# Kernel optimization log

Measured on AMD Instinct MI355X. Metric: run time of the kernel, lower is better.

Reference implementation:

```python
import jax, jax.numpy as jnp
import numpy as np

B, N, C, CP, H, NQ, NK = 1, 2048, 128, 16, 8, 32, 128
DH = C // H
PAD = NK // 2 - NQ // 2  # 48
NB = N // NQ  # 64 windows


def _ln(x, gamma=None, beta=None, eps=1e-5):
    mu = jnp.mean(x, axis=-1, keepdims=True)
    var = jnp.var(x, axis=-1, keepdims=True)
    y = (x - mu) * jax.lax.rsqrt(var + eps)
    if gamma is not None:
        y = y * gamma
    if beta is not None:
        y = y + beta
    return y


def _forward(atom_single_repr, atom_single_proj, atom_pair_repr,
             gamma_s, Wg_ada, bg_ada, W_skip,
             gamma_p, beta_p, W_pair,
             Wq, Wk, Wv, Wg, bg, Wo, bo, W_out, b_out):
    # --- AdaLN(a, s): LN(a) modulated by s ---
    a_ln = _ln(atom_single_repr)                       # no affine
    s_ln = _ln(atom_single_proj, gamma_s)              # scale only
    a = jax.nn.sigmoid(s_ln @ Wg_ada + bg_ada) * a_ln + s_ln @ W_skip  # (B,N,C)

    # --- pair bias: LN + no-bias linear to heads ---
    pair_bias = _ln(atom_pair_repr, gamma_p, beta_p) @ W_pair          # (B,N,N,H)

    # --- extract_local_biases: pad key dim with -10000, take sliding blocks ---
    pb = jnp.pad(pair_bias, ((0, 0), (0, 0), (PAD, PAD), (0, 0)),
                 constant_values=-10000.0)                              # (B,N,N+2P,H)
    rows = pb.reshape(B, NB, NQ, N + 2 * PAD, H)
    col_idx = (jnp.arange(NB) * NQ)[:, None] + jnp.arange(NK)[None, :]  # (NB,NK)
    local_bias = jnp.take_along_axis(rows, col_idx[None, :, None, :, None], axis=3)
    bias = jnp.transpose(local_bias, (0, 1, 4, 2, 3))                   # (B,NB,H,NQ,NK)

    # --- partition_tensor for queries (stride==size, no pad) and keys/values ---
    q_x = a.reshape(B, NB, NQ, C)
    a_pad = jnp.pad(a, ((0, 0), (PAD, PAD), (0, 0)))
    kv_x = a_pad[:, col_idx, :]                                         # (B,NB,NK,C)

    # --- OpenFold-style gated attention per window ---
    q = (q_x @ Wq).reshape(B, NB, NQ, H, DH) * (DH ** -0.5)
    k = (kv_x @ Wk).reshape(B, NB, NK, H, DH)
    v = (kv_x @ Wv).reshape(B, NB, NK, H, DH)
    logits = jnp.einsum('bwqhd,bwkhd->bwhqk', q, k) + bias
    attn = jax.nn.softmax(logits, axis=-1)
    o = jnp.einsum('bwhqk,bwkhd->bwqhd', attn, v).reshape(B, NB, NQ, C)
    g = jax.nn.sigmoid(q_x @ Wg + bg)
    o = (o * g) @ Wo + bo                                               # (B,NB,NQ,C)
    out = o.reshape(B, N, C)

    # --- output gating ---
    return jax.nn.sigmoid(out @ W_out + b_out) * out


def setup_inputs() -> dict:
    key = jax.random.key(0)
    ks = jax.random.split(key, 16)
    s = 0.02
    return {
        'atom_single_repr': jax.random.normal(ks[0], (B, N, C), jnp.float32),
        'atom_single_proj': jax.random.normal(ks[1], (B, N, C), jnp.float32),
        'atom_pair_repr': jax.random.normal(ks[2], (B, N, N, CP), jnp.float32),
        'gamma_s': jnp.ones((C,), jnp.float32),
        'Wg_ada': s * jax.random.normal(ks[3], (C, C), jnp.float32),
        'bg_ada': jnp.zeros((C,), jnp.float32),
        'W_skip': s * jax.random.normal(ks[4], (C, C), jnp.float32),
        'gamma_p': jnp.ones((CP,), jnp.float32),
        'beta_p': jnp.zeros((CP,), jnp.float32),
        'W_pair': s * jax.random.normal(ks[5], (CP, H), jnp.float32),
        'Wq': s * jax.random.normal(ks[6], (C, C), jnp.float32),
        'Wk': s * jax.random.normal(ks[7], (C, C), jnp.float32),
        'Wv': s * jax.random.normal(ks[8], (C, C), jnp.float32),
        'Wg': s * jax.random.normal(ks[9], (C, C), jnp.float32),
        'bg': jnp.ones((C,), jnp.float32),
        'Wo': s * jax.random.normal(ks[10], (C, C), jnp.float32),
        'bo': jnp.zeros((C,), jnp.float32),
        'W_out': s * jax.random.normal(ks[11], (C, C), jnp.float32),
        'b_out': -2.0 * jnp.ones((C,), jnp.float32),
    }


def reference(atom_single_repr, atom_single_proj, atom_pair_repr,
              gamma_s, Wg_ada, bg_ada, W_skip, gamma_p, beta_p, W_pair,
              Wq, Wk, Wv, Wg, bg, Wo, bo, W_out, b_out):
    return _forward(atom_single_repr, atom_single_proj, atom_pair_repr,
                    gamma_s, Wg_ada, bg_ada, W_skip, gamma_p, beta_p, W_pair,
                    Wq, Wk, Wv, Wg, bg, Wo, bo, W_out, b_out)
```

## Files before the change

kernel.cpp:

```cpp
#include <hip/hip_runtime.h>
#include <math.h>

#define NTOK 2048
#define CC   128
#define CPP  16
#define HH   8
#define DHH  16
#define NQW  32
#define NKW  128
#define PADW 48
#define NBW  64

__device__ __forceinline__ float sigm(float x) { return 1.0f / (1.0f + expf(-x)); }

__global__ __launch_bounds__(256) void k1_fused(
    const float* __restrict__ x1, const float* __restrict__ x2,
    const float* __restrict__ gamma_s,
    const float* __restrict__ Wg_ada, const float* __restrict__ bg_ada,
    const float* __restrict__ W_skip,
    const float* __restrict__ Wq, const float* __restrict__ Wk,
    const float* __restrict__ Wv, const float* __restrict__ Wg,
    const float* __restrict__ bg,
    const float* __restrict__ pair,
    const float* __restrict__ gamma_p, const float* __restrict__ beta_p,
    const float* __restrict__ W_pair,
    float* __restrict__ qb, float* __restrict__ kb,
    float* __restrict__ vb, float* __restrict__ gb,
    float* __restrict__ bias)
{
  const int b   = blockIdx.x;
  const int tid = threadIdx.x;

  if (b < 256) {
    __shared__ float sln[8][132];
    __shared__ float aln[8][132];
    __shared__ float as_[8][132];
    const int r0 = b * 8;

    {
      const int r = tid >> 5, t = tid & 31, c0 = t * 4;
      const int row = r0 + r;
      float4 v1 = *(const float4*)(x1 + (size_t)row * CC + c0);
      float4 v2 = *(const float4*)(x2 + (size_t)row * CC + c0);
      float s1 = v1.x + v1.y + v1.z + v1.w;
      float p1 = v1.x * v1.x + v1.y * v1.y + v1.z * v1.z + v1.w * v1.w;
      float s2 = v2.x + v2.y + v2.z + v2.w;
      float p2 = v2.x * v2.x + v2.y * v2.y + v2.z * v2.z + v2.w * v2.w;
#pragma unroll
      for (int m = 1; m < 32; m <<= 1) {
        s1 += __shfl_xor(s1, m); p1 += __shfl_xor(p1, m);
        s2 += __shfl_xor(s2, m); p2 += __shfl_xor(p2, m);
      }
      const float rc = 1.0f / 128.0f;
      float mu1 = s1 * rc, mu2 = s2 * rc;
      float rs1 = rsqrtf(p1 * rc - mu1 * mu1 + 1e-5f);
      float rs2 = rsqrtf(p2 * rc - mu2 * mu2 + 1e-5f);
      float4 gs = *(const float4*)(gamma_s + c0);
      float4 al, sl;
      al.x = (v1.x - mu1) * rs1; al.y = (v1.y - mu1) * rs1;
      al.z = (v1.z - mu1) * rs1; al.w = (v1.w - mu1) * rs1;
      sl.x = (v2.x - mu2) * rs2 * gs.x; sl.y = (v2.y - mu2) * rs2 * gs.y;
      sl.z = (v2.z - mu2) * rs2 * gs.z; sl.w = (v2.w - mu2) * rs2 * gs.w;
      *(float4*)(&aln[r][c0]) = al;
      *(float4*)(&sln[r][c0]) = sl;
    }
    __syncthreads();

    {
      const int rh = tid >> 7, cg = tid & 127;
      float g0 = 0.f, g1 = 0.f, g2 = 0.f, g3 = 0.f;
      float s0 = 0.f, s1 = 0.f, s2 = 0.f, s3 = 0.f;
#pragma unroll 4
      for (int k4 = 0; k4 < 32; ++k4) {
        float4 a0 = *(const float4*)(&sln[rh * 4 + 0][k4 * 4]);
        float4 a1 = *(const float4*)(&sln[rh * 4 + 1][k4 * 4]);
        float4 a2 = *(const float4*)(&sln[rh * 4 + 2][k4 * 4]);
        float4 a3 = *(const float4*)(&sln[rh * 4 + 3][k4 * 4]);
#define S1STEP(AX, J) { \
        float wg = Wg_ada[(k4 * 4 + J) * CC + cg]; \
        float wk = W_skip[(k4 * 4 + J) * CC + cg]; \
        g0 = fmaf(a0.AX, wg, g0); g1 = fmaf(a1.AX, wg, g1); \
        g2 = fmaf(a2.AX, wg, g2); g3 = fmaf(a3.AX, wg, g3); \
        s0 = fmaf(a0.AX, wk, s0); s1 = fmaf(a1.AX, wk, s1); \
        s2 = fmaf(a2.AX, wk, s2); s3 = fmaf(a3.AX, wk, s3); }
        S1STEP(x, 0) S1STEP(y, 1) S1STEP(z, 2) S1STEP(w, 3)
#undef S1STEP
      }
      float bga = bg_ada[cg];
      as_[rh * 4 + 0][cg] = sigm(g0 + bga) * aln[rh * 4 + 0][cg] + s0;
      as_[rh * 4 + 1][cg] = sigm(g1 + bga) * aln[rh * 4 + 1][cg] + s1;
      as_[rh * 4 + 2][cg] = sigm(g2 + bga) * aln[rh * 4 + 2][cg] + s2;
      as_[rh * 4 + 3][cg] = sigm(g3 + bga) * aln[rh * 4 + 3][cg] + s3;
    }
    __syncthreads();

    {
      const int m  = tid >> 6;
      const int l  = tid & 63;
      const int c0 = l * 2;
      const float* Wm = (m == 0) ? Wq : (m == 1) ? Wk : (m == 2) ? Wv : Wg;
      float2 c0_ = {0.f, 0.f}, c1_ = {0.f, 0.f}, c2_ = {0.f, 0.f}, c3_ = {0.f, 0.f};
      float2 c4_ = {0.f, 0.f}, c5_ = {0.f, 0.f}, c6_ = {0.f, 0.f}, c7_ = {0.f, 0.f};
#pragma unroll 2
      for (int k4 = 0; k4 < 32; ++k4) {
        float4 ra0 = *(const float4*)(&as_[0][k4 * 4]);
        float4 ra1 = *(const float4*)(&as_[1][k4 * 4]);
        float4 ra2 = *(const float4*)(&as_[2][k4 * 4]);
        float4 ra3 = *(const float4*)(&as_[3][k4 * 4]);
        float4 ra4 = *(const float4*)(&as_[4][k4 * 4]);
        float4 ra5 = *(const float4*)(&as_[5][k4 * 4]);
        float4 ra6 = *(const float4*)(&as_[6][k4 * 4]);
        float4 ra7 = *(const float4*)(&as_[7][k4 * 4]);
#define PJSTEP(AX, J) { \
        float2 wv = *(const float2*)(Wm + (k4 * 4 + J) * CC + c0); \
        c0_.x = fmaf(ra0.AX, wv.x, c0_.x); c0_.y = fmaf(ra0.AX, wv.y, c0_.y); \
        c1_.x = fmaf(ra1.AX, wv.x, c1_.x); c1_.y = fmaf(ra1.AX, wv.y, c1_.y); \
        c2_.x = fmaf(ra2.AX, wv.x, c2_.x); c2_.y = fmaf(ra2.AX, wv.y, c2_.y); \
        c3_.x = fmaf(ra3.AX, wv.x, c3_.x); c3_.y = fmaf(ra3.AX, wv.y, c3_.y); \
        c4_.x = fmaf(ra4.AX, wv.x, c4_.x); c4_.y = fmaf(ra4.AX, wv.y, c4_.y); \
        c5_.x = fmaf(ra5.AX, wv.x, c5_.x); c5_.y = fmaf(ra5.AX, wv.y, c5_.y); \
        c6_.x = fmaf(ra6.AX, wv.x, c6_.x); c6_.y = fmaf(ra6.AX, wv.y, c6_.y); \
        c7_.x = fmaf(ra7.AX, wv.x, c7_.x); c7_.y = fmaf(ra7.AX, wv.y, c7_.y); }
        PJSTEP(x, 0) PJSTEP(y, 1) PJSTEP(z, 2) PJSTEP(w, 3)
#undef PJSTEP
      }
      if (m == 0) {
#define QST(I, CI) { float2 r; r.x = CI.x * 0.25f; r.y = CI.y * 0.25f; \
        *(float2*)(qb + (size_t)(r0 + I) * CC + c0) = r; }
        QST(0, c0_) QST(1, c1_) QST(2, c2_) QST(3, c3_)
        QST(4, c4_) QST(5, c5_) QST(6, c6_) QST(7, c7_)
#undef QST
      } else if (m == 1) {
#define KST(I, CI) *(float2*)(kb + (size_t)(r0 + I) * CC + c0) = CI;
        KST(0, c0_) KST(1, c1_) KST(2, c2_) KST(3, c3_)
        KST(4, c4_) KST(5, c5_) KST(6, c6_) KST(7, c7_)
#undef KST
      } else if (m == 2) {
#define VST(I, CI) *(float2*)(vb + (size_t)(r0 + I) * CC + c0) = CI;
        VST(0, c0_) VST(1, c1_) VST(2, c2_) VST(3, c3_)
        VST(4, c4_) VST(5, c5_) VST(6, c6_) VST(7, c7_)
#undef VST
      } else {
        float2 bgv = *(const float2*)(bg + c0);
#define GST(I, CI) { float2 r; r.x = sigm(CI.x + bgv.x); r.y = sigm(CI.y + bgv.y); \
        *(float2*)(gb + (size_t)(r0 + I) * CC + c0) = r; }
        GST(0, c0_) GST(1, c1_) GST(2, c2_) GST(3, c3_)
        GST(4, c4_) GST(5, c5_) GST(6, c6_) GST(7, c7_)
#undef GST
      }
    }
  } else {
    __shared__ float wp[CPP * HH];
    __shared__ float gp[CPP];
    __shared__ float bp[CPP];
    if (tid < CPP * HH) wp[tid] = W_pair[tid];
    if (tid < CPP) { gp[tid] = gamma_p[tid]; bp[tid] = beta_p[tid]; }
    __syncthreads();

    const int i  = (b - 256) * 2 + (tid >> 7);
    const int w  = i >> 5;
    const int qq = i & 31;
    const int k  = tid & 127;
    const int j  = w * NQW + k - PADW;

    float bh[HH];
    if (j >= 0 && j < NTOK) {
      const float* p = pair + ((size_t)i * NTOK + j) * CPP;
      float x[CPP];
#pragma unroll
      for (int u = 0; u < CPP; u += 4) {
        float4 v = *(const float4*)(p + u);
        x[u] = v.x; x[u + 1] = v.y; x[u + 2] = v.z; x[u + 3] = v.w;
      }
      float s = 0.f;
#pragma unroll
      for (int c = 0; c < CPP; ++c) s += x[c];
      float mu = s * (1.0f / CPP);
      float vv = 0.f;
#pragma unroll
      for (int c = 0; c < CPP; ++c) { float d = x[c] - mu; vv = fmaf(d, d, vv); }
      float rs = rsqrtf(vv * (1.0f / CPP) + 1e-5f);
#pragma unroll
      for (int h = 0; h < HH; ++h) bh[h] = 0.f;
#pragma unroll
      for (int c = 0; c < CPP; ++c) {
        float y = (x[c] - mu) * rs * gp[c] + bp[c];
#pragma unroll
        for (int h = 0; h < HH; ++h) bh[h] = fmaf(y, wp[c * HH + h], bh[h]);
      }
    } else {
#pragma unroll
      for (int h = 0; h < HH; ++h) bh[h] = -10000.0f;
    }
#pragma unroll
    for (int h = 0; h < HH; ++h)
      bias[((size_t)((w * HH + h) * NQW + qq)) * NKW + k] = bh[h];
  }
}

__global__ __launch_bounds__(256) void attn_kernel(
    const float* __restrict__ qb, const float* __restrict__ kb,
    const float* __restrict__ vb, const float* __restrict__ bias,
    float* __restrict__ ob)
{
  __shared__ float qs[16][20];
  __shared__ float ks[NKW][20];
  __shared__ float vs[NKW][20];
  __shared__ float bs[16][132];
  const int u   = blockIdx.x;
  const int w   = u >> 4;
  const int h   = (u >> 1) & 7;
  const int qh  = u & 1;
  const int tid = threadIdx.x;

  if (tid < 64) {
    int qr = tid >> 2, c4 = (tid & 3) * 4;
    float4 v = *(const float4*)(qb + (size_t)(w * NQW + qh * 16 + qr) * CC + h * DHH + c4);
    *(float4*)(&qs[qr][c4]) = v;
  }
  {
    int kr = tid >> 1, c8 = (tid & 1) * 8;
    int j = w * NQW + kr - PADW;
    float4 k0 = make_float4(0.f, 0.f, 0.f, 0.f), k1 = k0, v0 = k0, v1 = k0;
    if (j >= 0 && j < NTOK) {
      const float* kp = kb + (size_t)j * CC + h * DHH + c8;
      const float* vp = vb + (size_t)j * CC + h * DHH + c8;
      k0 = *(const float4*)(kp);     k1 = *(const float4*)(kp + 4);
      v0 = *(const float4*)(vp);     v1 = *(const float4*)(vp + 4);
    }
    *(float4*)(&ks[kr][c8])     = k0;
    *(float4*)(&ks[kr][c8 + 4]) = k1;
    *(float4*)(&vs[kr][c8])     = v0;
    *(float4*)(&vs[kr][c8 + 4]) = v1;
  }
  {
    const float* bt = bias + (size_t)(w * HH + h) * NQW * NKW + (size_t)qh * 16 * NKW;
    int qr = tid >> 4, k8 = (tid & 15) * 8;
    float4 b0 = *(const float4*)(bt + qr * NKW + k8);
    float4 b1 = *(const float4*)(bt + qr * NKW + k8 + 4);
    *(float4*)(&bs[qr][k8])     = b0;
    *(float4*)(&bs[qr][k8 + 4]) = b1;
  }
  __syncthreads();

  const int qr = tid >> 4;
  const int t  = tid & 15;
  float4 q0 = *(float4*)(&qs[qr][0]);
  float4 q1 = *(float4*)(&qs[qr][4]);
  float4 q2 = *(float4*)(&qs[qr][8]);
  float4 q3 = *(float4*)(&qs[qr][12]);

  float l[8];
#pragma unroll
  for (int i = 0; i < 8; ++i) {
    int k = t + 16 * i;
    const float* kr_ = &ks[k][0];
    float4 k0 = *(const float4*)(kr_);
    float4 k1 = *(const float4*)(kr_ + 4);
    float4 k2 = *(const float4*)(kr_ + 8);
    float4 k3 = *(const float4*)(kr_ + 12);
    float d = 0.f;
    d = fmaf(q0.x, k0.x, d); d = fmaf(q0.y, k0.y, d);
    d = fmaf(q0.z, k0.z, d); d = fmaf(q0.w, k0.w, d);
    d = fmaf(q1.x, k1.x, d); d = fmaf(q1.y, k1.y, d);
    d = fmaf(q1.z, k1.z, d); d = fmaf(q1.w, k1.w, d);
    d = fmaf(q2.x, k2.x, d); d = fmaf(q2.y, k2.y, d);
    d = fmaf(q2.z, k2.z, d); d = fmaf(q2.w, k2.w, d);
    d = fmaf(q3.x, k3.x, d); d = fmaf(q3.y, k3.y, d);
    d = fmaf(q3.z, k3.z, d); d = fmaf(q3.w, k3.w, d);
    l[i] = d + bs[qr][k];
  }

  float m0 = l[0];
#pragma unroll
  for (int i = 1; i < 8; ++i) m0 = fmaxf(m0, l[i]);
  m0 = fmaxf(m0, __shfl_xor(m0, 1));
  m0 = fmaxf(m0, __shfl_xor(m0, 2));
  m0 = fmaxf(m0, __shfl_xor(m0, 4));
  m0 = fmaxf(m0, __shfl_xor(m0, 8));
  float s = 0.f;
  float p[8];
#pragma unroll
  for (int i = 0; i < 8; ++i) { p[i] = expf(l[i] - m0); s += p[i]; }
  s += __shfl_xor(s, 1);
  s += __shfl_xor(s, 2);
  s += __shfl_xor(s, 4);
  s += __shfl_xor(s, 8);
  float inv = 1.0f / s;
#pragma unroll
  for (int i = 0; i < 8; ++i) p[i] *= inv;

  float o[16];
#pragma unroll
  for (int d = 0; d < 16; ++d) o[d] = 0.f;
#pragma unroll
  for (int i = 0; i < 8; ++i) {
    int k = t + 16 * i;
    const float* vr = &vs[k][0];
    float4 v0 = *(const float4*)(vr);
    float4 v1 = *(const float4*)(vr + 4);
    float4 v2 = *(const float4*)(vr + 8);
    float4 v3 = *(const float4*)(vr + 12);
    float pa = p[i];
    o[0]  = fmaf(pa, v0.x, o[0]);  o[1]  = fmaf(pa, v0.y, o[1]);
    o[2]  = fmaf(pa, v0.z, o[2]);  o[3]  = fmaf(pa, v0.w, o[3]);
    o[4]  = fmaf(pa, v1.x, o[4]);  o[5]  = fmaf(pa, v1.y, o[5]);
    o[6]  = fmaf(pa, v1.z, o[6]);  o[7]  = fmaf(pa, v1.w, o[7]);
    o[8]  = fmaf(pa, v2.x, o[8]);  o[9]  = fmaf(pa, v2.y, o[9]);
    o[10] = fmaf(pa, v2.z, o[10]); o[11] = fmaf(pa, v2.w, o[11]);
    o[12] = fmaf(pa, v3.x, o[12]); o[13] = fmaf(pa, v3.y, o[13]);
    o[14] = fmaf(pa, v3.z, o[14]); o[15] = fmaf(pa, v3.w, o[15]);
  }
#pragma unroll
  for (int d = 0; d < 16; ++d) {
#pragma unroll
    for (int m = 1; m < 16; m <<= 1) o[d] += __shfl_xor(o[d], m);
  }
  float wsel = 0.f;
#pragma unroll
  for (int d = 0; d < 16; ++d) wsel = (t == d) ? o[d] : wsel;
  ob[(size_t)(w * NQW + qh * 16 + qr) * CC + h * DHH + t] = wsel;
}

__global__ __launch_bounds__(256) void k3_out(
    const float* __restrict__ ob_, const float* __restrict__ gb_,
    const float* __restrict__ Wo, const float* __restrict__ bo,
    const float* __restrict__ W_out, const float* __restrict__ b_out,
    float* __restrict__ out)
{
  __shared__ float og[8][132];
  __shared__ float us[8][132];
  const int r0  = blockIdx.x * 8;
  const int tid = threadIdx.x;
  {
    const int r = tid >> 5, t = tid & 31, c0 = t * 4;
    float4 o4 = *(const float4*)(ob_ + (size_t)(r0 + r) * CC + c0);
    float4 g4 = *(const float4*)(gb_ + (size_t)(r0 + r) * CC + c0);
    float4 m4;
    m4.x = o4.x * g4.x; m4.y = o4.y * g4.y;
    m4.z = o4.z * g4.z; m4.w = o4.w * g4.w;
    *(float4*)(&og[r][c0]) = m4;
  }
  __syncthreads();

  const int rh = tid >> 7, cg = tid & 127;
  float u0 = 0.f, u1 = 0.f, u2 = 0.f, u3 = 0.f;
#pragma unroll 4
  for (int k4 = 0; k4 < 32; ++k4) {
    float4 a0 = *(const float4*)(&og[rh * 4 + 0][k4 * 4]);
    float4 a1 = *(const float4*)(&og[rh * 4 + 1][k4 * 4]);
    float4 a2 = *(const float4*)(&og[rh * 4 + 2][k4 * 4]);
    float4 a3 = *(const float4*)(&og[rh * 4 + 3][k4 * 4]);
#define O1STEP(AX, J) { \
    float wv = Wo[(k4 * 4 + J) * CC + cg]; \
    u0 = fmaf(a0.AX, wv, u0); u1 = fmaf(a1.AX, wv, u1); \
    u2 = fmaf(a2.AX, wv, u2); u3 = fmaf(a3.AX, wv, u3); }
    O1STEP(x, 0) O1STEP(y, 1) O1STEP(z, 2) O1STEP(w, 3)
#undef O1STEP
  }
  float bov = bo[cg];
  u0 += bov; u1 += bov; u2 += bov; u3 += bov;
  us[rh * 4 + 0][cg] = u0;
  us[rh * 4 + 1][cg] = u1;
  us[rh * 4 + 2][cg] = u2;
  us[rh * 4 + 3][cg] = u3;
  __syncthreads();

  float a0s = 0.f, a1s = 0.f, a2s = 0.f, a3s = 0.f;
#pragma unroll 4
  for (int k4 = 0; k4 < 32; ++k4) {
    float4 a0 = *(const float4*)(&us[rh * 4 + 0][k4 * 4]);
    float4 a1 = *(const float4*)(&us[rh * 4 + 1][k4 * 4]);
    float4 a2 = *(const float4*)(&us[rh * 4 + 2][k4 * 4]);
    float4 a3 = *(const float4*)(&us[rh * 4 + 3][k4 * 4]);
#define O2STEP(AX, J) { \
    float wv = W_out[(k4 * 4 + J) * CC + cg]; \
    a0s = fmaf(a0.AX, wv, a0s); a1s = fmaf(a1.AX, wv, a1s); \
    a2s = fmaf(a2.AX, wv, a2s); a3s = fmaf(a3.AX, wv, a3s); }
    O2STEP(x, 0) O2STEP(y, 1) O2STEP(z, 2) O2STEP(w, 3)
#undef O2STEP
  }
  float b2 = b_out[cg];
  out[(size_t)(r0 + rh * 4 + 0) * CC + cg] = sigm(a0s + b2) * u0;
  out[(size_t)(r0 + rh * 4 + 1) * CC + cg] = sigm(a1s + b2) * u1;
  out[(size_t)(r0 + rh * 4 + 2) * CC + cg] = sigm(a2s + b2) * u2;
  out[(size_t)(r0 + rh * 4 + 3) * CC + cg] = sigm(a3s + b2) * u3;
}

extern "C" void kernel_launch(void* const* d_in, const int* in_sizes, int n_in,
                              void* d_out, int out_size, void* d_ws, size_t ws_size,
                              hipStream_t stream) {
  (void)in_sizes; (void)n_in; (void)out_size; (void)ws_size;
  const float* x1      = (const float*)d_in[0];
  const float* x2      = (const float*)d_in[1];
  const float* pair    = (const float*)d_in[2];
  const float* gamma_s = (const float*)d_in[3];
  const float* Wg_ada  = (const float*)d_in[4];
  const float* bg_ada  = (const float*)d_in[5];
  const float* W_skip  = (const float*)d_in[6];
  const float* gamma_p = (const float*)d_in[7];
  const float* beta_p  = (const float*)d_in[8];
  const float* W_pair  = (const float*)d_in[9];
  const float* Wq      = (const float*)d_in[10];
  const float* Wk      = (const float*)d_in[11];
  const float* Wv      = (const float*)d_in[12];
  const float* Wg      = (const float*)d_in[13];
  const float* bg      = (const float*)d_in[14];
  const float* Wo      = (const float*)d_in[15];
  const float* bo      = (const float*)d_in[16];
  const float* W_out   = (const float*)d_in[17];
  const float* b_out   = (const float*)d_in[18];

  float* ws   = (float*)d_ws;
  const size_t NC = (size_t)NTOK * CC;
  float* qb   = ws;
  float* kb   = ws + NC;
  float* vb   = ws + 2 * NC;
  float* gb   = ws + 3 * NC;
  float* obuf = ws + 4 * NC;
  float* bias = ws + 5 * NC;

  k1_fused<<<1280, 256, 0, stream>>>(x1, x2, gamma_s, Wg_ada, bg_ada, W_skip,
                                     Wq, Wk, Wv, Wg, bg,
                                     pair, gamma_p, beta_p, W_pair,
                                     qb, kb, vb, gb, bias);
  attn_kernel<<<1024, 256, 0, stream>>>(qb, kb, vb, bias, obuf);
  k3_out<<<256, 256, 0, stream>>>(obuf, gb, Wo, bo, W_out, b_out,
                                  (float*)d_out);
}
```

Baseline: 45.07 us.

## Merge three kernels into one cooperative persistent kernel with grid syncs

Replaces the three launches (projection/bias, windowed attention, output projection) with a single cooperative kernel of 512 blocks that separates phases with grid.sync(). Each block now handles several bias rows and two attention units per phase, and shared memory is unioned across phases. The aim is to remove launch gaps and inter-kernel drain, at the cost of grid-wide barriers, fewer blocks per phase and launch_bounds(256,2) register limits.

```diff
diff --git a/kernel.cpp b/kernel.cpp
--- a/kernel.cpp
+++ b/kernel.cpp
@@ -1,5 +1,8 @@
 #include <hip/hip_runtime.h>
+#include <hip/hip_cooperative_groups.h>
 #include <math.h>
+
+namespace cg = cooperative_groups;
 
 #define NTOK 2048
 #define CC   128
@@ -13,35 +16,33 @@
 
 __device__ __forceinline__ float sigm(float x) { return 1.0f / (1.0f + expf(-x)); }
 
-__global__ __launch_bounds__(256) void k1_fused(
-    const float* __restrict__ x1, const float* __restrict__ x2,
-    const float* __restrict__ gamma_s,
-    const float* __restrict__ Wg_ada, const float* __restrict__ bg_ada,
-    const float* __restrict__ W_skip,
-    const float* __restrict__ Wq, const float* __restrict__ Wk,
-    const float* __restrict__ Wv, const float* __restrict__ Wg,
-    const float* __restrict__ bg,
-    const float* __restrict__ pair,
-    const float* __restrict__ gamma_p, const float* __restrict__ beta_p,
-    const float* __restrict__ W_pair,
-    float* __restrict__ qb, float* __restrict__ kb,
-    float* __restrict__ vb, float* __restrict__ gb,
-    float* __restrict__ bias)
-{
+struct Params {
+  const float *x1, *x2, *gamma_s, *Wg_ada, *bg_ada, *W_skip;
+  const float *Wq, *Wk, *Wv, *Wg, *bg;
+  const float *pair, *gamma_p, *beta_p, *W_pair;
+  const float *Wo, *bo, *W_out, *b_out;
+  float *qb, *kb, *vb, *gb, *obuf, *bias, *out;
+};
+
+__global__ __launch_bounds__(256, 2) void mega_kernel(Params P) {
+  union SMem {
+    struct { float sln[8][132], aln[8][132], as_[8][132]; } prep;
+    struct { float wp[CPP * HH], gp[CPP], bp[CPP]; } bia;
+    struct { float qs[16][20], ks[NKW][20], vs[NKW][20], bs[16][132]; } at;
+    struct { float og[4][132], us[4][132]; } outp;
+  };
+  __shared__ SMem sm;
+  cg::grid_group grid = cg::this_grid();
   const int b   = blockIdx.x;
   const int tid = threadIdx.x;
 
   if (b < 256) {
-    __shared__ float sln[8][132];
-    __shared__ float aln[8][132];
-    __shared__ float as_[8][132];
     const int r0 = b * 8;
-
     {
       const int r = tid >> 5, t = tid & 31, c0 = t * 4;
       const int row = r0 + r;
-      float4 v1 = *(const float4*)(x1 + (size_t)row * CC + c0);
-      float4 v2 = *(const float4*)(x2 + (size_t)row * CC + c0);
+      float4 v1 = *(const float4*)(P.x1 + (size_t)row * CC + c0);
+      float4 v2 = *(const float4*)(P.x2 + (size_t)row * CC + c0);
       float s1 = v1.x + v1.y + v1.z + v1.w;
       float p1 = v1.x * v1.x + v1.y * v1.y + v1.z * v1.z + v1.w * v1.w;
       float s2 = v2.x + v2.y + v2.z + v2.w;
@@ -55,14 +56,14 @@
       float mu1 = s1 * rc, mu2 = s2 * rc;
       float rs1 = rsqrtf(p1 * rc - mu1 * mu1 + 1e-5f);
       float rs2 = rsqrtf(p2 * rc - mu2 * mu2 + 1e-5f);
-      float4 gs = *(const float4*)(gamma_s + c0);
+      float4 gs = *(const float4*)(P.gamma_s + c0);
       float4 al, sl;
       al.x = (v1.x - mu1) * rs1; al.y = (v1.y - mu1) * rs1;
       al.z = (v1.z - mu1) * rs1; al.w = (v1.w - mu1) * rs1;
       sl.x = (v2.x - mu2) * rs2 * gs.x; sl.y = (v2.y - mu2) * rs2 * gs.y;
       sl.z = (v2.z - mu2) * rs2 * gs.z; sl.w = (v2.w - mu2) * rs2 * gs.w;
-      *(float4*)(&aln[r][c0]) = al;
-      *(float4*)(&sln[r][c0]) = sl;
+      *(float4*)(&sm.prep.aln[r][c0]) = al;
+      *(float4*)(&sm.prep.sln[r][c0]) = sl;
     }
     __syncthreads();
 
@@ -72,13 +73,13 @@
       float s0 = 0.f, s1 = 0.f, s2 = 0.f, s3 = 0.f;
 #pragma unroll 4
       for (int k4 = 0; k4 < 32; ++k4) {
-        float4 a0 = *(const float4*)(&sln[rh * 4 + 0][k4 * 4]);
-        float4 a1 = *(const float4*)(&sln[rh * 4 + 1][k4 * 4]);
-        float4 a2 = *(const float4*)(&sln[rh * 4 + 2][k4 * 4]);
-        float4 a3 = *(const float4*)(&sln[rh * 4 + 3][k4 * 4]);
+        float4 a0 = *(const float4*)(&sm.prep.sln[rh * 4 + 0][k4 * 4]);
+        float4 a1 = *(const float4*)(&sm.prep.sln[rh * 4 + 1][k4 * 4]);
+        float4 a2 = *(const float4*)(&sm.prep.sln[rh * 4 + 2][k4 * 4]);
+        float4 a3 = *(const float4*)(&sm.prep.sln[rh * 4 + 3][k4 * 4]);
 #define S1STEP(AX, J) { \
-        float wg = Wg_ada[(k4 * 4 + J) * CC + cg]; \
-        float wk = W_skip[(k4 * 4 + J) * CC + cg]; \
+        float wg = P.Wg_ada[(k4 * 4 + J) * CC + cg]; \
+        float wk = P.W_skip[(k4 * 4 + J) * CC + cg]; \
         g0 = fmaf(a0.AX, wg, g0); g1 = fmaf(a1.AX, wg, g1); \
         g2 = fmaf(a2.AX, wg, g2); g3 = fmaf(a3.AX, wg, g3); \
         s0 = fmaf(a0.AX, wk, s0); s1 = fmaf(a1.AX, wk, s1); \
@@ -86,11 +87,16 @@
         S1STEP(x, 0) S1STEP(y, 1) S1STEP(z, 2) S1STEP(w, 3)
 #undef S1STEP
       }
-      float bga = bg_ada[cg];
-      as_[rh * 4 + 0][cg] = sigm(g0 + bga) * aln[rh * 4 + 0][cg] + s0;
-      as_[rh * 4 + 1][cg] = sigm(g1 + bga) * aln[rh * 4 + 1][cg] + s1;
-      as_[rh * 4 + 2][cg] = sigm(g2 + bga) * aln[rh * 4 + 2][cg] + s2;
-      as_[rh * 4 + 3][cg] = sigm(g3 + bga) * aln[rh * 4 + 3][cg] + s3;
+      float bga = P.bg_ada[cg];
+      float o0 = sigm(g0 + bga) * sm.prep.aln[rh * 4 + 0][cg] + s0;
+      float o1 = sigm(g1 + bga) * sm.prep.aln[rh * 4 + 1][cg] + s1;
+      float o2 = sigm(g2 + bga) * sm.prep.aln[rh * 4 + 2][cg] + s2;
+      float o3 = sigm(g3 + bga) * sm.prep.aln[rh * 4 + 3][cg] + s3;
+      __syncthreads();
+      sm.prep.as_[rh * 4 + 0][cg] = o0;
+      sm.prep.as_[rh * 4 + 1][cg] = o1;
+      sm.prep.as_[rh * 4 + 2][cg] = o2;
+      sm.prep.as_[rh * 4 + 3][cg] = o3;
     }
     __syncthreads();
 
@@ -98,19 +104,19 @@
       const int m  = tid >> 6;
       const int l  = tid & 63;
       const int c0 = l * 2;
-      const float* Wm = (m == 0) ? Wq : (m == 1) ? Wk : (m == 2) ? Wv : Wg;
+      const float* Wm = (m == 0) ? P.Wq : (m == 1) ? P.Wk : (m == 2) ? P.Wv : P.Wg;
       float2 c0_ = {0.f, 0.f}, c1_ = {0.f, 0.f}, c2_ = {0.f, 0.f}, c3_ = {0.f, 0.f};
       float2 c4_ = {0.f, 0.f}, c5_ = {0.f, 0.f}, c6_ = {0.f, 0.f}, c7_ = {0.f, 0.f};
 #pragma unroll 2
       for (int k4 = 0; k4 < 32; ++k4) {
-        float4 ra0 = *(const float4*)(&as_[0][k4 * 4]);
-        float4 ra1 = *(const float4*)(&as_[1][k4 * 4]);
-        float4 ra2 = *(const float4*)(&as_[2][k4 * 4]);
-        float4 ra3 = *(const float4*)(&as_[3][k4 * 4]);
-        float4 ra4 = *(const float4*)(&as_[4][k4 * 4]);
-        float4 ra5 = *(const float4*)(&as_[5][k4 * 4]);
-        float4 ra6 = *(const float4*)(&as_[6][k4 * 4]);
-        float4 ra7 = *(const float4*)(&as_[7][k4 * 4]);
+        float4 ra0 = *(const float4*)(&sm.prep.as_[0][k4 * 4]);
+        float4 ra1 = *(const float4*)(&sm.prep.as_[1][k4 * 4]);
+        float4 ra2 = *(const float4*)(&sm.prep.as_[2][k4 * 4]);
+        float4 ra3 = *(const float4*)(&sm.prep.as_[3][k4 * 4]);
+        float4 ra4 = *(const float4*)(&sm.prep.as_[4][k4 * 4]);
+        float4 ra5 = *(const float4*)(&sm.prep.as_[5][k4 * 4]);
+        float4 ra6 = *(const float4*)(&sm.prep.as_[6][k4 * 4]);
+        float4 ra7 = *(const float4*)(&sm.prep.as_[7][k4 * 4]);
 #define PJSTEP(AX, J) { \
         float2 wv = *(const float2*)(Wm + (k4 * 4 + J) * CC + c0); \
         c0_.x = fmaf(ra0.AX, wv.x, c0_.x); c0_.y = fmaf(ra0.AX, wv.y, c0_.y); \
@@ -126,305 +132,281 @@
       }
       if (m == 0) {
 #define QST(I, CI) { float2 r; r.x = CI.x * 0.25f; r.y = CI.y * 0.25f; \
-        *(float2*)(qb + (size_t)(r0 + I) * CC + c0) = r; }
+        *(float2*)(P.qb + (size_t)(r0 + I) * CC + c0) = r; }
         QST(0, c0_) QST(1, c1_) QST(2, c2_) QST(3, c3_)
         QST(4, c4_) QST(5, c5_) QST(6, c6_) QST(7, c7_)
 #undef QST
       } else if (m == 1) {
-#define KST(I, CI) *(float2*)(kb + (size_t)(r0 + I) * CC + c0) = CI;
+#define KST(I, CI) *(float2*)(P.kb + (size_t)(r0 + I) * CC + c0) = CI;
         KST(0, c0_) KST(1, c1_) KST(2, c2_) KST(3, c3_)
         KST(4, c4_) KST(5, c5_) KST(6, c6_) KST(7, c7_)
 #undef KST
       } else if (m == 2) {
-#define VST(I, CI) *(float2*)(vb + (size_t)(r0 + I) * CC + c0) = CI;
+#define VST(I, CI) *(float2*)(P.vb + (size_t)(r0 + I) * CC + c0) = CI;
         VST(0, c0_) VST(1, c1_) VST(2, c2_) VST(3, c3_)
         VST(4, c4_) VST(5, c5_) VST(6, c6_) VST(7, c7_)
 #undef VST
       } else {
-        float2 bgv = *(const float2*)(bg + c0);
+        float2 bgv = *(const float2*)(P.bg + c0);
 #define GST(I, CI) { float2 r; r.x = sigm(CI.x + bgv.x); r.y = sigm(CI.y + bgv.y); \
-        *(float2*)(gb + (size_t)(r0 + I) * CC + c0) = r; }
+        *(float2*)(P.gb + (size_t)(r0 + I) * CC + c0) = r; }
         GST(0, c0_) GST(1, c1_) GST(2, c2_) GST(3, c3_)
         GST(4, c4_) GST(5, c5_) GST(6, c6_) GST(7, c7_)
 #undef GST
       }
     }
   } else {
-    __shared__ float wp[CPP * HH];
-    __shared__ float gp[CPP];
-    __shared__ float bp[CPP];
-    if (tid < CPP * HH) wp[tid] = W_pair[tid];
-    if (tid < CPP) { gp[tid] = gamma_p[tid]; bp[tid] = beta_p[tid]; }
-    __syncthreads();
-
-    const int i  = (b - 256) * 2 + (tid >> 7);
-    const int w  = i >> 5;
-    const int qq = i & 31;
-    const int k  = tid & 127;
-    const int j  = w * NQW + k - PADW;
-
-    float bh[HH];
-    if (j >= 0 && j < NTOK) {
-      const float* p = pair + ((size_t)i * NTOK + j) * CPP;
-      float x[CPP];
-#pragma unroll
-      for (int u = 0; u < CPP; u += 4) {
-        float4 v = *(const float4*)(p + u);
-        x[u] = v.x; x[u + 1] = v.y; x[u + 2] = v.z; x[u + 3] = v.w;
-      }
-      float s = 0.f;
-#pragma unroll
-      for (int c = 0; c < CPP; ++c) s += x[c];
-      float mu = s * (1.0f / CPP);
-      float vv = 0.f;
-#pragma unroll
-      for (int c = 0; c < CPP; ++c) { float d = x[c] - mu; vv = fmaf(d, d, vv); }
-      float rs = rsqrtf(vv * (1.0f / CPP) + 1e-5f);
-#pragma unroll
-      for (int h = 0; h < HH; ++h) bh[h] = 0.f;
-#pragma unroll
-      for (int c = 0; c < CPP; ++c) {
-        float y = (x[c] - mu) * rs * gp[c] + bp[c];
-#pragma unroll
-        for (int h = 0; h < HH; ++h) bh[h] = fmaf(y, wp[c * HH + h], bh[h]);
-      }
-    } else {
-#pragma unroll
-      for (int h = 0; h < HH; ++h) bh[h] = -10000.0f;
-    }
-#pragma unroll
-    for (int h = 0; h < HH; ++h)
-      bias[((size_t)((w * HH + h) * NQW + qq)) * NKW + k] = bh[h];
+    if (tid < CPP * HH) sm.bia.wp[tid] = P.W_pair[tid];
+    if (tid < CPP) { sm.bia.gp[tid] = P.gamma_p[tid]; sm.bia.bp[tid] = P.beta_p[tid]; }
+    __syncthreads();
+
+#pragma unroll
+    for (int it = 0; it < 4; ++it) {
+      const int i  = (b - 256) * 8 + it * 2 + (tid >> 7);
+      const int w  = i >> 5;
+      const int qq = i & 31;
+      const int k  = tid & 127;
+      const int j  = w * NQW + k - PADW;
+
+      float bh[HH];
+      if (j >= 0 && j < NTOK) {
+        const float* p = P.pair + ((size_t)i * NTOK + j) * CPP;
+        float x[CPP];
+#pragma unroll
+        for (int u4 = 0; u4 < CPP; u4 += 4) {
+          float4 v = *(const float4*)(p + u4);
+          x[u4] = v.x; x[u4 + 1] = v.y; x[u4 + 2] = v.z; x[u4 + 3] = v.w;
+        }
+        float s = 0.f;
+#pragma unroll
+        for (int c = 0; c < CPP; ++c) s += x[c];
+        float mu = s * (1.0f / CPP);
+        float vv = 0.f;
+#pragma unroll
+        for (int c = 0; c < CPP; ++c) { float d = x[c] - mu; vv = fmaf(d, d, vv); }
+        float rs = rsqrtf(vv * (1.0f / CPP) + 1e-5f);
+#pragma unroll
+        for (int h = 0; h < HH; ++h) bh[h] = 0.f;
+#pragma unroll
+        for (int c = 0; c < CPP; ++c) {
+          float y = (x[c] - mu) * rs * sm.bia.gp[c] + sm.bia.bp[c];
+#pragma unroll
+          for (int h = 0; h < HH; ++h) bh[h] = fmaf(y, sm.bia.wp[c * HH + h], bh[h]);
+        }
+      } else {
+#pragma unroll
+        for (int h = 0; h < HH; ++h) bh[h] = -10000.0f;
+      }
+#pragma unroll
+      for (int h = 0; h < HH; ++h)
+        P.bias[((size_t)((w * HH + h) * NQW + qq)) * NKW + k] = bh[h];
+    }
   }
-}
-
-__global__ __launch_bounds__(256) void attn_kernel(
-    const float* __restrict__ qb, const float* __restrict__ kb,
-    const float* __restrict__ vb, const float* __restrict__ bias,
-    float* __restrict__ ob)
-{
-  __shared__ float qs[16][20];
-  __shared__ float ks[NKW][20];
-  __shared__ float vs[NKW][20];
-  __shared__ float bs[16][132];
-  const int u   = blockIdx.x;
-  const int w   = u >> 4;
-  const int h   = (u >> 1) & 7;
-  const int qh  = u & 1;
-  const int tid = threadIdx.x;
-
-  if (tid < 64) {
-    int qr = tid >> 2, c4 = (tid & 3) * 4;
-    float4 v = *(const float4*)(qb + (size_t)(w * NQW + qh * 16 + qr) * CC + h * DHH + c4);
-    *(float4*)(&qs[qr][c4]) = v;
+
+  grid.sync();
+
+#pragma unroll 1
+  for (int rep = 0; rep < 2; ++rep) {
+    const int u  = b * 2 + rep;
+    const int w  = u >> 4;
+    const int h  = (u >> 1) & 7;
+    const int qh = u & 1;
+
+    if (tid < 64) {
+      int qr = tid >> 2, c4 = (tid & 3) * 4;
+      float4 v = *(const float4*)(P.qb + (size_t)(w * NQW + qh * 16 + qr) * CC + h * DHH + c4);
+      *(float4*)(&sm.at.qs[qr][c4]) = v;
+    }
+    {
+      int kr = tid >> 1, c8 = (tid & 1) * 8;
+      int j = w * NQW + kr - PADW;
+      float4 k0 = make_float4(0.f, 0.f, 0.f, 0.f), k1 = k0, v0 = k0, v1 = k0;
+      if (j >= 0 && j < NTOK) {
+        const float* kp = P.kb + (size_t)j * CC + h * DHH + c8;
+        const float* vp = P.vb + (size_t)j * CC + h * DHH + c8;
+        k0 = *(const float4*)(kp);     k1 = *(const float4*)(kp + 4);
+        v0 = *(const float4*)(vp);     v1 = *(const float4*)(vp + 4);
+      }
+      *(float4*)(&sm.at.ks[kr][c8])     = k0;
+      *(float4*)(&sm.at.ks[kr][c8 + 4]) = k1;
+      *(float4*)(&sm.at.vs[kr][c8])     = v0;
+      *(float4*)(&sm.at.vs[kr][c8 + 4]) = v1;
+    }
+    {
+      const float* bt = P.bias + (size_t)(w * HH + h) * NQW * NKW + (size_t)qh * 16 * NKW;
+      int qr = tid >> 4, k8 = (tid & 15) * 8;
+      float4 b0 = *(const float4*)(bt + qr * NKW + k8);
+      float4 b1 = *(const float4*)(bt + qr * NKW + k8 + 4);
+      *(float4*)(&sm.at.bs[qr][k8])     = b0;
+      *(float4*)(&sm.at.bs[qr][k8 + 4]) = b1;
+    }
+    __syncthreads();
+
+    const int qr = tid >> 4;
+    const int t  = tid & 15;
+    float4 q0 = *(float4*)(&sm.at.qs[qr][0]);
+    float4 q1 = *(float4*)(&sm.at.qs[qr][4]);
+    float4 q2 = *(float4*)(&sm.at.qs[qr][8]);
+    float4 q3 = *(float4*)(&sm.at.qs[qr][12]);
+
+    float l[8];
+#pragma unroll
+    for (int i = 0; i < 8; ++i) {
+      int k = t + 16 * i;
+      const float* kr_ = &sm.at.ks[k][0];
+      float4 k0 = *(const float4*)(kr_);
+      float4 k1 = *(const float4*)(kr_ + 4);
+      float4 k2 = *(const float4*)(kr_ + 8);
+      float4 k3 = *(const float4*)(kr_ + 12);
+      float d = 0.f;
+      d = fmaf(q0.x, k0.x, d); d = fmaf(q0.y, k0.y, d);
+      d = fmaf(q0.z, k0.z, d); d = fmaf(q0.w, k0.w, d);
+      d = fmaf(q1.x, k1.x, d); d = fmaf(q1.y, k1.y, d);
+      d = fmaf(q1.z, k1.z, d); d = fmaf(q1.w, k1.w, d);
+      d = fmaf(q2.x, k2.x, d); d = fmaf(q2.y, k2.y, d);
+      d = fmaf(q2.z, k2.z, d); d = fmaf(q2.w, k2.w, d);
+      d = fmaf(q3.x, k3.x, d); d = fmaf(q3.y, k3.y, d);
+      d = fmaf(q3.z, k3.z, d); d = fmaf(q3.w, k3.w, d);
+      l[i] = d + sm.at.bs[qr][k];
+    }
+
+    float m0 = l[0];
+#pragma unroll
+    for (int i = 1; i < 8; ++i) m0 = fmaxf(m0, l[i]);
+    m0 = fmaxf(m0, __shfl_xor(m0, 1));
+    m0 = fmaxf(m0, __shfl_xor(m0, 2));
+    m0 = fmaxf(m0, __shfl_xor(m0, 4));
+    m0 = fmaxf(m0, __shfl_xor(m0, 8));
+    float s = 0.f;
+    float p[8];
+#pragma unroll
+    for (int i = 0; i < 8; ++i) { p[i] = expf(l[i] - m0); s += p[i]; }
+    s += __shfl_xor(s, 1);
+    s += __shfl_xor(s, 2);
+    s += __shfl_xor(s, 4);
+    s += __shfl_xor(s, 8);
+    float inv = 1.0f / s;
+#pragma unroll
+    for (int i = 0; i < 8; ++i) p[i] *= inv;
+
+    float o[16];
+#pragma unroll
+    for (int d = 0; d < 16; ++d) o[d] = 0.f;
+#pragma unroll
+    for (int i = 0; i < 8; ++i) {
+      int k = t + 16 * i;
+      const float* vr = &sm.at.vs[k][0];
+      float4 v0 = *(const float4*)(vr);
+      float4 v1 = *(const float4*)(vr + 4);
+      float4 v2 = *(const float4*)(vr + 8);
+      float4 v3 = *(const float4*)(vr + 12);
+      float pa = p[i];
+      o[0]  = fmaf(pa, v0.x, o[0]);  o[1]  = fmaf(pa, v0.y, o[1]);
+      o[2]  = fmaf(pa, v0.z, o[2]);  o[3]  = fmaf(pa, v0.w, o[3]);
+      o[4]  = fmaf(pa, v1.x, o[4]);  o[5]  = fmaf(pa, v1.y, o[5]);
+      o[6]  = fmaf(pa, v1.z, o[6]);  o[7]  = fmaf(pa, v1.w, o[7]);
+      o[8]  = fmaf(pa, v2.x, o[8]);  o[9]  = fmaf(pa, v2.y, o[9]);
+      o[10] = fmaf(pa, v2.z, o[10]); o[11] = fmaf(pa, v2.w, o[11]);
+      o[12] = fmaf(pa, v3.x, o[12]); o[13] = fmaf(pa, v3.y, o[13]);
+      o[14] = fmaf(pa, v3.z, o[14]); o[15] = fmaf(pa, v3.w, o[15]);
+    }
+#pragma unroll
+    for (int d = 0; d < 16; ++d) {
+#pragma unroll
+      for (int m = 1; m < 16; m <<= 1) o[d] += __shfl_xor(o[d], m);
+    }
+    float wsel = 0.f;
+#pragma unroll
+    for (int d = 0; d < 16; ++d) wsel = (t == d) ? o[d] : wsel;
+    P.obuf[(size_t)(w * NQW + qh * 16 + qr) * CC + h * DHH + t] = wsel;
+    __syncthreads();
   }
+
+  grid.sync();
+
   {
-    int kr = tid >> 1, c8 = (tid & 1) * 8;
-    int j = w * NQW + kr - PADW;
-    float4 k0 = make_float4(0.f, 0.f, 0.f, 0.f), k1 = k0, v0 = k0, v1 = k0;
-    if (j >= 0 && j < NTOK) {
-      const float* kp = kb + (size_t)j * CC + h * DHH + c8;
-      const float* vp = vb + (size_t)j * CC + h * DHH + c8;
-      k0 = *(const float4*)(kp);     k1 = *(const float4*)(kp + 4);
-      v0 = *(const float4*)(vp);     v1 = *(const float4*)(vp + 4);
-    }
-    *(float4*)(&ks[kr][c8])     = k0;
-    *(float4*)(&ks[kr][c8 + 4]) = k1;
-    *(float4*)(&vs[kr][c8])     = v0;
-    *(float4*)(&vs[kr][c8 + 4]) = v1;
+    const int r0 = b * 4;
+    {
+      const int r = tid >> 6, t = tid & 63, c0 = t * 2;
+      float2 o2 = *(const float2*)(P.obuf + (size_t)(r0 + r) * CC + c0);
+      float2 g2 = *(const float2*)(P.gb   + (size_t)(r0 + r) * CC + c0);
+      sm.outp.og[r][c0]     = o2.x * g2.x;
+      sm.outp.og[r][c0 + 1] = o2.y * g2.y;
+    }
+    __syncthreads();
+
+    const int rh = tid >> 7, cg = tid & 127;
+    const int ra = rh * 2, rb = rh * 2 + 1;
+    float u0 = 0.f, u1 = 0.f;
+#pragma unroll 4
+    for (int k4 = 0; k4 < 32; ++k4) {
+      float4 a0 = *(const float4*)(&sm.outp.og[ra][k4 * 4]);
+      float4 a1 = *(const float4*)(&sm.outp.og[rb][k4 * 4]);
+#define C1STEP(AX, J) { \
+      float wv = P.Wo[(k4 * 4 + J) * CC + cg]; \
+      u0 = fmaf(a0.AX, wv, u0); u1 = fmaf(a1.AX, wv, u1); }
+      C1STEP(x, 0) C1STEP(y, 1) C1STEP(z, 2) C1STEP(w, 3)
+#undef C1STEP
+    }
+    float bov = P.bo[cg];
+    u0 += bov; u1 += bov;
+    sm.outp.us[ra][cg] = u0;
+    sm.outp.us[rb][cg] = u1;
+    __syncthreads();
+
+    float a0s = 0.f, a1s = 0.f;
+#pragma unroll 4
+    for (int k4 = 0; k4 < 32; ++k4) {
+      float4 a0 = *(const float4*)(&sm.outp.us[ra][k4 * 4]);
+      float4 a1 = *(const float4*)(&sm.outp.us[rb][k4 * 4]);
+#define C2STEP(AX, J) { \
+      float wv = P.W_out[(k4 * 4 + J) * CC + cg]; \
+      a0s = fmaf(a0.AX, wv, a0s); a1s = fmaf(a1.AX, wv, a1s); }
+      C2STEP(x, 0) C2STEP(y, 1) C2STEP(z, 2) C2STEP(w, 3)
+#undef C2STEP
+    }
+    float b2 = P.b_out[cg];
+    P.out[(size_t)(r0 + ra) * CC + cg] = sigm(a0s + b2) * u0;
+    P.out[(size_t)(r0 + rb) * CC + cg] = sigm(a1s + b2) * u1;
   }
-  {
-    const float* bt = bias + (size_t)(w * HH + h) * NQW * NKW + (size_t)qh * 16 * NKW;
-    int qr = tid >> 4, k8 = (tid & 15) * 8;
-    float4 b0 = *(const float4*)(bt + qr * NKW + k8);
-    float4 b1 = *(const float4*)(bt + qr * NKW + k8 + 4);
-    *(float4*)(&bs[qr][k8])     = b0;
-    *(float4*)(&bs[qr][k8 + 4]) = b1;
-  }
-  __syncthreads();
-
-  const int qr = tid >> 4;
-  const int t  = tid & 15;
-  float4 q0 = *(float4*)(&qs[qr][0]);
-  float4 q1 = *(float4*)(&qs[qr][4]);
-  float4 q2 = *(float4*)(&qs[qr][8]);
-  float4 q3 = *(float4*)(&qs[qr][12]);
-
-  float l[8];
-#pragma unroll
-  for (int i = 0; i < 8; ++i) {
-    int k = t + 16 * i;
-    const float* kr_ = &ks[k][0];
-    float4 k0 = *(const float4*)(kr_);
-    float4 k1 = *(const float4*)(kr_ + 4);
-    float4 k2 = *(const float4*)(kr_ + 8);
-    float4 k3 = *(const float4*)(kr_ + 12);
-    float d = 0.f;
-    d = fmaf(q0.x, k0.x, d); d = fmaf(q0.y, k0.y, d);
-    d = fmaf(q0.z, k0.z, d); d = fmaf(q0.w, k0.w, d);
-    d = fmaf(q1.x, k1.x, d); d = fmaf(q1.y, k1.y, d);
-    d = fmaf(q1.z, k1.z, d); d = fmaf(q1.w, k1.w, d);
-    d = fmaf(q2.x, k2.x, d); d = fmaf(q2.y, k2.y, d);
-    d = fmaf(q2.z, k2.z, d); d = fmaf(q2.w, k2.w, d);
-    d = fmaf(q3.x, k3.x, d); d = fmaf(q3.y, k3.y, d);
-    d = fmaf(q3.z, k3.z, d); d = fmaf(q3.w, k3.w, d);
-    l[i] = d + bs[qr][k];
-  }
-
-  float m0 = l[0];
-#pragma unroll
-  for (int i = 1; i < 8; ++i) m0 = fmaxf(m0, l[i]);
-  m0 = fmaxf(m0, __shfl_xor(m0, 1));
-  m0 = fmaxf(m0, __shfl_xor(m0, 2));
-  m0 = fmaxf(m0, __shfl_xor(m0, 4));
-  m0 = fmaxf(m0, __shfl_xor(m0, 8));
-  float s = 0.f;
-  float p[8];
-#pragma unroll
-  for (int i = 0; i < 8; ++i) { p[i] = expf(l[i] - m0); s += p[i]; }
-  s += __shfl_xor(s, 1);
-  s += __shfl_xor(s, 2);
-  s += __shfl_xor(s, 4);
-  s += __shfl_xor(s, 8);
-  float inv = 1.0f / s;
-#pragma unroll
-  for (int i = 0; i < 8; ++i) p[i] *= inv;
-
-  float o[16];
-#pragma unroll
-  for (int d = 0; d < 16; ++d) o[d] = 0.f;
-#pragma unroll
-  for (int i = 0; i < 8; ++i) {
-    int k = t + 16 * i;
-    const float* vr = &vs[k][0];
-    float4 v0 = *(const float4*)(vr);
-    float4 v1 = *(const float4*)(vr + 4);
-    float4 v2 = *(const float4*)(vr + 8);
-    float4 v3 = *(const float4*)(vr + 12);
-    float pa = p[i];
-    o[0]  = fmaf(pa, v0.x, o[0]);  o[1]  = fmaf(pa, v0.y, o[1]);
-    o[2]  = fmaf(pa, v0.z, o[2]);  o[3]  = fmaf(pa, v0.w, o[3]);
-    o[4]  = fmaf(pa, v1.x, o[4]);  o[5]  = fmaf(pa, v1.y, o[5]);
-    o[6]  = fmaf(pa, v1.z, o[6]);  o[7]  = fmaf(pa, v1.w, o[7]);
-    o[8]  = fmaf(pa, v2.x, o[8]);  o[9]  = fmaf(pa, v2.y, o[9]);
-    o[10] = fmaf(pa, v2.z, o[10]); o[11] = fmaf(pa, v2.w, o[11]);
-    o[12] = fmaf(pa, v3.x, o[12]); o[13] = fmaf(pa, v3.y, o[13]);
-    o[14] = fmaf(pa, v3.z, o[14]); o[15] = fmaf(pa, v3.w, o[15]);
-  }
-#pragma unroll
-  for (int d = 0; d < 16; ++d) {
-#pragma unroll
-    for (int m = 1; m < 16; m <<= 1) o[d] += __shfl_xor(o[d], m);
-  }
-  float wsel = 0.f;
-#pragma unroll
-  for (int d = 0; d < 16; ++d) wsel = (t == d) ? o[d] : wsel;
-  ob[(size_t)(w * NQW + qh * 16 + qr) * CC + h * DHH + t] = wsel;
-}
-
-__global__ __launch_bounds__(256) void k3_out(
-    const float* __restrict__ ob_, const float* __restrict__ gb_,
-    const float* __restrict__ Wo, const float* __restrict__ bo,
-    const float* __restrict__ W_out, const float* __restrict__ b_out,
-    float* __restrict__ out)
-{
-  __shared__ float og[8][132];
-  __shared__ float us[8][132];
-  const int r0  = blockIdx.x * 8;
-  const int tid = threadIdx.x;
-  {
-    const int r = tid >> 5, t = tid & 31, c0 = t * 4;
-    float4 o4 = *(const float4*)(ob_ + (size_t)(r0 + r) * CC + c0);
-    float4 g4 = *(const float4*)(gb_ + (size_t)(r0 + r) * CC + c0);
-    float4 m4;
-    m4.x = o4.x * g4.x; m4.y = o4.y * g4.y;
-    m4.z = o4.z * g4.z; m4.w = o4.w * g4.w;
-    *(float4*)(&og[r][c0]) = m4;
-  }
-  __syncthreads();
-
-  const int rh = tid >> 7, cg = tid & 127;
-  float u0 = 0.f, u1 = 0.f, u2 = 0.f, u3 = 0.f;
-#pragma unroll 4
-  for (int k4 = 0; k4 < 32; ++k4) {
-    float4 a0 = *(const float4*)(&og[rh * 4 + 0][k4 * 4]);
-    float4 a1 = *(const float4*)(&og[rh * 4 + 1][k4 * 4]);
-    float4 a2 = *(const float4*)(&og[rh * 4 + 2][k4 * 4]);
-    float4 a3 = *(const float4*)(&og[rh * 4 + 3][k4 * 4]);
-#define O1STEP(AX, J) { \
-    float wv = Wo[(k4 * 4 + J) * CC + cg]; \
-    u0 = fmaf(a0.AX, wv, u0); u1 = fmaf(a1.AX, wv, u1); \
-    u2 = fmaf(a2.AX, wv, u2); u3 = fmaf(a3.AX, wv, u3); }
-    O1STEP(x, 0) O1STEP(y, 1) O1STEP(z, 2) O1STEP(w, 3)
-#undef O1STEP
-  }
-  float bov = bo[cg];
-  u0 += bov; u1 += bov; u2 += bov; u3 += bov;
-  us[rh * 4 + 0][cg] = u0;
-  us[rh * 4 + 1][cg] = u1;
-  us[rh * 4 + 2][cg] = u2;
-  us[rh * 4 + 3][cg] = u3;
-  __syncthreads();
-
-  float a0s = 0.f, a1s = 0.f, a2s = 0.f, a3s = 0.f;
-#pragma unroll 4
-  for (int k4 = 0; k4 < 32; ++k4) {
-    float4 a0 = *(const float4*)(&us[rh * 4 + 0][k4 * 4]);
-    float4 a1 = *(const float4*)(&us[rh * 4 + 1][k4 * 4]);
-    float4 a2 = *(const float4*)(&us[rh * 4 + 2][k4 * 4]);
-    float4 a3 = *(const float4*)(&us[rh * 4 + 3][k4 * 4]);
-#define O2STEP(AX, J) { \
-    float wv = W_out[(k4 * 4 + J) * CC + cg]; \
-    a0s = fmaf(a0.AX, wv, a0s); a1s = fmaf(a1.AX, wv, a1s); \
-    a2s = fmaf(a2.AX, wv, a2s); a3s = fmaf(a3.AX, wv, a3s); }
-    O2STEP(x, 0) O2STEP(y, 1) O2STEP(z, 2) O2STEP(w, 3)
-#undef O2STEP
-  }
-  float b2 = b_out[cg];
-  out[(size_t)(r0 + rh * 4 + 0) * CC + cg] = sigm(a0s + b2) * u0;
-  out[(size_t)(r0 + rh * 4 + 1) * CC + cg] = sigm(a1s + b2) * u1;
-  out[(size_t)(r0 + rh * 4 + 2) * CC + cg] = sigm(a2s + b2) * u2;
-  out[(size_t)(r0 + rh * 4 + 3) * CC + cg] = sigm(a3s + b2) * u3;
 }
 
 extern "C" void kernel_launch(void* const* d_in, const int* in_sizes, int n_in,
                               void* d_out, int out_size, void* d_ws, size_t ws_size,
                               hipStream_t stream) {
   (void)in_sizes; (void)n_in; (void)out_size; (void)ws_size;
-  const float* x1      = (const float*)d_in[0];
-  const float* x2      = (const float*)d_in[1];
-  const float* pair    = (const float*)d_in[2];
-  const float* gamma_s = (const float*)d_in[3];
-  const float* Wg_ada  = (const float*)d_in[4];
-  const float* bg_ada  = (const float*)d_in[5];
-  const float* W_skip  = (const float*)d_in[6];
-  const float* gamma_p = (const float*)d_in[7];
-  const float* beta_p  = (const float*)d_in[8];
-  const float* W_pair  = (const float*)d_in[9];
-  const float* Wq      = (const float*)d_in[10];
-  const float* Wk      = (const float*)d_in[11];
-  const float* Wv      = (const float*)d_in[12];
-  const float* Wg      = (const float*)d_in[13];
-  const float* bg      = (const float*)d_in[14];
-  const float* Wo      = (const float*)d_in[15];
-  const float* bo      = (const float*)d_in[16];
-  const float* W_out   = (const float*)d_in[17];
-  const float* b_out   = (const float*)d_in[18];
-
-  float* ws   = (float*)d_ws;
+  float* ws = (float*)d_ws;
   const size_t NC = (size_t)NTOK * CC;
-  float* qb   = ws;
-  float* kb   = ws + NC;
-  float* vb   = ws + 2 * NC;
-  float* gb   = ws + 3 * NC;
-  float* obuf = ws + 4 * NC;
-  float* bias = ws + 5 * NC;
-
-  k1_fused<<<1280, 256, 0, stream>>>(x1, x2, gamma_s, Wg_ada, bg_ada, W_skip,
-                                     Wq, Wk, Wv, Wg, bg,
-                                     pair, gamma_p, beta_p, W_pair,
-                                     qb, kb, vb, gb, bias);
-  attn_kernel<<<1024, 256, 0, stream>>>(qb, kb, vb, bias, obuf);
-  k3_out<<<256, 256, 0, stream>>>(obuf, gb, Wo, bo, W_out, b_out,
-                                  (float*)d_out);
+
+  Params P;
+  P.x1      = (const float*)d_in[0];
+  P.x2      = (const float*)d_in[1];
+  P.pair    = (const float*)d_in[2];
+  P.gamma_s = (const float*)d_in[3];
+  P.Wg_ada  = (const float*)d_in[4];
+  P.bg_ada  = (const float*)d_in[5];
+  P.W_skip  = (const float*)d_in[6];
+  P.gamma_p = (const float*)d_in[7];
+  P.beta_p  = (const float*)d_in[8];
+  P.W_pair  = (const float*)d_in[9];
+  P.Wq      = (const float*)d_in[10];
+  P.Wk      = (const float*)d_in[11];
+  P.Wv      = (const float*)d_in[12];
+  P.Wg      = (const float*)d_in[13];
+  P.bg      = (const float*)d_in[14];
+  P.Wo      = (const float*)d_in[15];
+  P.bo      = (const float*)d_in[16];
+  P.W_out   = (const float*)d_in[17];
+  P.b_out   = (const float*)d_in[18];
+  P.qb   = ws;
+  P.kb   = ws + NC;
+  P.vb   = ws + 2 * NC;
+  P.gb   = ws + 3 * NC;
+  P.obuf = ws + 4 * NC;
+  P.bias = ws + 5 * NC;
+  P.out  = (float*)d_out;
+
+  void* kargs[] = { (void*)&P };
+  hipLaunchCooperativeKernel((const void*)mega_kernel, dim3(512), dim3(256),
+                             kargs, 0, stream);
 }
```

New measurement: 159.7 us. +254.3%, slower.
